# Performance work log

Hardware: AMD Instinct MI355X
Metric: run time of the kernel (lower is better)

The kernel has to match this reference:

```python
import jax, jax.numpy as jnp
import numpy as np

HUGE = 1e31  # ops.HUGE_INT
EPS = 1e-20

NUM_ENT, NUM_REL = 100000, 400
ENT_D, REL_D, HIST_D = 256, 256, 512
ACT_D = ENT_D + REL_D          # 512
IN_D = ENT_D + HIST_D + REL_D  # 1024
B, A = 512, 256


def setup_inputs() -> dict:
    key = jax.random.key(0)
    ks = jax.random.split(key, 10)
    s = 0.02
    return {
        "current_entity": jax.random.randint(ks[0], (B,), 0, NUM_ENT),
        "query_relation": jax.random.randint(ks[1], (B,), 0, NUM_REL),
        "encoded_history": jax.random.normal(ks[2], (B, HIST_D), jnp.float32),
        "r_space": jax.random.randint(ks[3], (B, A), 0, NUM_REL),
        "e_space": jax.random.randint(ks[4], (B, A), 0, NUM_ENT),
        "action_mask": jax.random.randint(ks[5], (B, A), 0, 2).astype(jnp.int32),
        "entity_emb": jax.random.normal(ks[6], (NUM_ENT, ENT_D), jnp.float32) * s,
        "relation_emb": jax.random.normal(ks[7], (NUM_REL, REL_D), jnp.float32) * s,
        "W1": jax.random.normal(ks[8], (IN_D, ACT_D), jnp.float32) * s,
        "b1": jnp.zeros((ACT_D,), jnp.float32),
        "W2": jax.random.normal(ks[9], (ACT_D, ACT_D), jnp.float32) * s,
        "b2": jnp.zeros((ACT_D,), jnp.float32),
    }


def reference(current_entity, query_relation, encoded_history, r_space, e_space,
              action_mask, entity_emb, relation_emb, W1, b1, W2, b2):
    # encode_history: [E(cur) | lstm hidden | R(query)] -> [B, IN_D]
    X = jnp.concatenate([entity_emb[current_entity], encoded_history,
                         relation_emb[query_relation]], axis=-1)
    # policy MLP (dropout = identity in eval)
    X2 = jax.nn.relu(X @ W1 + b1) @ W2 + b2          # [B, ACT_D]
    # per-action embeddings: concat(rel, ent) -> [B, A, ACT_D]
    A_emb = jnp.concatenate([relation_emb[r_space], entity_emb[e_space]], axis=-1)
    mask = action_mask.astype(X2.dtype)
    scores = jnp.einsum('bad,bd->ba', A_emb, X2) - (1.0 - mask) * HUGE
    action_dist = jax.nn.softmax(scores, axis=-1)    # [B, A]
    entropy = -jnp.sum(action_dist * jnp.log(action_dist + EPS), axis=-1)  # [B]
    return action_dist, entropy
```

## Files before the change

kernel.cpp:

```cpp
#include <hip/hip_runtime.h>
#include <hip/hip_bf16.h>

#define ENT_D 256
#define REL_D 256
#define HIST_D 512
#define ACT_DD 512
#define IN_DD 1024
#define BB 512
#define AA 256

typedef short bf16x8 __attribute__((ext_vector_type(8)));
typedef float floatx4 __attribute__((ext_vector_type(4)));

__device__ __forceinline__ unsigned short f2bf(float f) {
    unsigned u = __builtin_bit_cast(unsigned, f);
    return (unsigned short)((u + 0x7fffu + ((u >> 16) & 1u)) >> 16);
}


__global__ __launch_bounds__(256) void pack_kernel(
    const int* __restrict__ cur, const int* __restrict__ qrel,
    const float* __restrict__ hist,
    const float* __restrict__ ent_emb, const float* __restrict__ rel_emb,
    const float* __restrict__ W1, const float* __restrict__ W2,
    unsigned short* __restrict__ W1p, unsigned short* __restrict__ W2p,
    unsigned short* __restrict__ Xp)
{
    const int wid  = blockIdx.x * 4 + (threadIdx.x >> 6);
    const int lane = threadIdx.x & 63;
    const int l15  = lane & 15;
    const int quad = lane >> 4;
    unsigned short v[8];

    if (wid < 1024) {
        const int t = wid, nt = t >> 5, kt = t & 31;
        const int n = nt * 16 + l15, k0 = kt * 32 + quad * 8;
#pragma unroll
        for (int j = 0; j < 8; ++j) v[j] = f2bf(W1[(size_t)(k0 + j) * ACT_DD + n]);
        *(bf16x8*)(W1p + ((size_t)t * 64 + lane) * 8) = *(bf16x8*)v;
    } else if (wid < 1536) {
        const int t = wid - 1024, nt = t >> 4, kt = t & 15;
        const int n = nt * 16 + l15, k0 = kt * 32 + quad * 8;
#pragma unroll
        for (int j = 0; j < 8; ++j) v[j] = f2bf(W2[(size_t)(k0 + j) * ACT_DD + n]);
        *(bf16x8*)(W2p + ((size_t)t * 64 + lane) * 8) = *(bf16x8*)v;
    } else {
        const int t = wid - 1536, mt = t >> 5, kt = t & 31;
        const int m = mt * 16 + l15, k0 = kt * 32 + quad * 8;
        const float* src;
        if (k0 < ENT_D)            src = ent_emb + (size_t)cur[m] * ENT_D + k0;
        else if (k0 < ENT_D + HIST_D) src = hist + (size_t)m * HIST_D + (k0 - ENT_D);
        else                       src = rel_emb + (size_t)qrel[m] * REL_D + (k0 - ENT_D - HIST_D);
        float4 a = *(const float4*)src, b = *(const float4*)(src + 4);
        v[0]=f2bf(a.x); v[1]=f2bf(a.y); v[2]=f2bf(a.z); v[3]=f2bf(a.w);
        v[4]=f2bf(b.x); v[5]=f2bf(b.y); v[6]=f2bf(b.z); v[7]=f2bf(b.w);
        *(bf16x8*)(Xp + ((size_t)t * 64 + lane) * 8) = *(bf16x8*)v;
    }
}

__global__ __launch_bounds__(256) void gemm1_kernel(
    const unsigned short* __restrict__ Xp, const unsigned short* __restrict__ W1p,
    const float* __restrict__ b1, unsigned short* __restrict__ Hp)
{
    __shared__ unsigned short sH[1024];
    const int mt = blockIdx.x, wave = threadIdx.x >> 6, lane = threadIdx.x & 63;
    const int nt = blockIdx.y * 4 + wave;

    const bf16x8* Av = (const bf16x8*)Xp  + (size_t)mt * 32 * 64 + lane;
    const bf16x8* Bv = (const bf16x8*)W1p + (size_t)nt * 32 * 64 + lane;
    floatx4 acc = {0.f, 0.f, 0.f, 0.f};
#pragma unroll 8
    for (int kt = 0; kt < 32; ++kt)
        acc = __builtin_amdgcn_mfma_f32_16x16x32_bf16(Av[kt * 64], Bv[kt * 64], acc, 0, 0, 0);

    const int col  = nt * 16 + (lane & 15);
    const float bj = b1[col];
    const int n_loc = wave * 16 + (lane & 15);
    const int tile_loc = n_loc >> 5, quad2 = (n_loc & 31) >> 3, j2 = n_loc & 7;
#pragma unroll
    for (int reg = 0; reg < 4; ++reg) {
        const int row = (lane >> 4) * 4 + reg;
        const float h = fmaxf(acc[reg] + bj, 0.f);
        sH[tile_loc * 512 + (row + 16 * quad2) * 8 + j2] = f2bf(h);
    }
    __syncthreads();
    const int h = threadIdx.x * 4;
    const int tl = h >> 9, rest = h & 511;
    const size_t dst = ((size_t)(mt * 16 + blockIdx.y * 2 + tl) * 512 + rest);
    *(uint2*)(Hp + dst) = *(const uint2*)(sH + h);
}

__global__ __launch_bounds__(256) void gemm2_kernel(
    const unsigned short* __restrict__ Hp, const unsigned short* __restrict__ W2p,
    const float* __restrict__ b2, float* __restrict__ X2)
{
    const int mt = blockIdx.x, wave = threadIdx.x >> 6, lane = threadIdx.x & 63;
    const int nt = blockIdx.y * 4 + wave;

    const bf16x8* Av = (const bf16x8*)Hp  + (size_t)mt * 16 * 64 + lane;
    const bf16x8* Bv = (const bf16x8*)W2p + (size_t)nt * 16 * 64 + lane;
    floatx4 acc = {0.f, 0.f, 0.f, 0.f};
#pragma unroll
    for (int kt = 0; kt < 16; ++kt)
        acc = __builtin_amdgcn_mfma_f32_16x16x32_bf16(Av[kt * 64], Bv[kt * 64], acc, 0, 0, 0);

    const int col = nt * 16 + (lane & 15);
    const float bj = b2[col];
#pragma unroll
    for (int reg = 0; reg < 4; ++reg) {
        const int m = mt * 16 + (lane >> 4) * 4 + reg;
        X2[(size_t)m * ACT_DD + col] = acc[reg] + bj;
    }
}

__global__ __launch_bounds__(256) void score_kernel(
    const float* __restrict__ X2,
    const int* __restrict__ r_space, const int* __restrict__ e_space,
    const int* __restrict__ amask,
    const float* __restrict__ ent_emb, const float* __restrict__ rel_emb,
    float* __restrict__ scores)
{
    __shared__ __align__(16) float x2s[ACT_DD];
    const int b = blockIdx.x >> 2, chunk = blockIdx.x & 3;
    const int tid = threadIdx.x, wave = tid >> 6, lane = tid & 63;

    x2s[tid]       = X2[(size_t)b * ACT_DD + tid];
    x2s[tid + 256] = X2[(size_t)b * ACT_DD + tid + 256];
    __syncthreads();

    const float4 xr = ((const float4*)&x2s[0])[lane];
    const float4 xe = ((const float4*)&x2s[REL_D])[lane];
    const int a0 = chunk * 64 + wave * 16;

#pragma unroll
    for (int g = 0; g < 4; ++g) {
        const int ab = a0 + g * 4;
        int ir[4], ie[4];
        float p[4];
#pragma unroll
        for (int i = 0; i < 4; ++i) {
            ir[i] = r_space[b * AA + ab + i];
            ie[i] = e_space[b * AA + ab + i];
        }
#pragma unroll
        for (int i = 0; i < 4; ++i) {
            const float4 r4 = ((const float4*)(rel_emb + (size_t)ir[i] * REL_D))[lane];
            const float4 e4 = ((const float4*)(ent_emb + (size_t)ie[i] * ENT_D))[lane];
            p[i] = r4.x * xr.x + r4.y * xr.y + r4.z * xr.z + r4.w * xr.w
                 + e4.x * xe.x + e4.y * xe.y + e4.z * xe.z + e4.w * xe.w;
        }
#pragma unroll
        for (int off = 32; off > 0; off >>= 1) {
#pragma unroll
            for (int i = 0; i < 4; ++i) p[i] += __shfl_xor(p[i], off, 64);
        }
        if (lane == 0) {
#pragma unroll
            for (int i = 0; i < 4; ++i) {
                const float m = (float)amask[b * AA + ab + i];
                scores[(size_t)b * AA + ab + i] = p[i] - (1.0f - m) * 1e31f;
            }
        }
    }
}

__global__ __launch_bounds__(256) void softmax_kernel(
    const float* __restrict__ scores, float* __restrict__ dist, float* __restrict__ ent_out)
{
    __shared__ float red[4];
    const int b = blockIdx.x, tid = threadIdx.x, wave = tid >> 6, lane = tid & 63;
    const float s = scores[(size_t)b * AA + tid];

    float v = s;
#pragma unroll
    for (int off = 32; off > 0; off >>= 1) v = fmaxf(v, __shfl_xor(v, off, 64));
    if (lane == 0) red[wave] = v;
    __syncthreads();
    const float mx = fmaxf(fmaxf(red[0], red[1]), fmaxf(red[2], red[3]));
    __syncthreads();

    const float e = __expf(s - mx);
    v = e;
#pragma unroll
    for (int off = 32; off > 0; off >>= 1) v += __shfl_xor(v, off, 64);
    if (lane == 0) red[wave] = v;
    __syncthreads();
    const float sum = red[0] + red[1] + red[2] + red[3];
    __syncthreads();

    const float p = e / sum;
    dist[(size_t)b * AA + tid] = p;

    v = p * __logf(p + 1e-20f);
#pragma unroll
    for (int off = 32; off > 0; off >>= 1) v += __shfl_xor(v, off, 64);
    if (lane == 0) red[wave] = v;
    __syncthreads();
    if (tid == 0) ent_out[b] = -(red[0] + red[1] + red[2] + red[3]);
}

extern "C" void kernel_launch(void* const* d_in, const int* in_sizes, int n_in,
                              void* d_out, int out_size, void* d_ws, size_t ws_size,
                              hipStream_t stream) {
    const int*   cur      = (const int*)d_in[0];
    const int*   qrel     = (const int*)d_in[1];
    const float* hist     = (const float*)d_in[2];
    const int*   r_space  = (const int*)d_in[3];
    const int*   e_space  = (const int*)d_in[4];
    const int*   amask    = (const int*)d_in[5];
    const float* ent_emb  = (const float*)d_in[6];
    const float* rel_emb  = (const float*)d_in[7];
    const float* W1       = (const float*)d_in[8];
    const float* b1       = (const float*)d_in[9];
    const float* W2       = (const float*)d_in[10];
    const float* b2       = (const float*)d_in[11];

    float* dist    = (float*)d_out;
    float* entropy = dist + (size_t)BB * AA;

    char* w = (char*)d_ws;
    unsigned short* W1p = (unsigned short*)(w);
    unsigned short* W2p = (unsigned short*)(w + (1u << 20));
    unsigned short* Xp  = (unsigned short*)(w + (3u << 19));
    float*          scores = (float*)(w + (3u << 19));
    unsigned short* Hp  = (unsigned short*)(w + (5u << 19));
    float*          X2  = (float*)(w + (6u << 19));

    pack_kernel<<<640, 256, 0, stream>>>(cur, qrel, hist, ent_emb, rel_emb, W1, W2, W1p, W2p, Xp);
    gemm1_kernel<<<dim3(32, 8), 256, 0, stream>>>(Xp, W1p, b1, Hp);
    gemm2_kernel<<<dim3(32, 8), 256, 0, stream>>>(Hp, W2p, b2, X2);
    score_kernel<<<2048, 256, 0, stream>>>(X2, r_space, e_space, amask, ent_emb, rel_emb, scores);
    softmax_kernel<<<512, 256, 0, stream>>>(scores, dist, entropy);
}
```

Before: 193.7 us.

## Fuse score gather and softmax into one per-row kernel with deeper load batching

Merges the score and softmax kernels into one kernel with one 512-thread block per batch row. Scores stay in shared memory instead of going out to a global buffer, which saves a kernel launch and a global round trip. Each wave now issues 8 rel and 8 ent row gathers before any arithmetic, so more memory requests are in flight. In exchange the grid shrinks from 2048 to 512 blocks and the softmax phase leaves half the threads idle.

```diff
diff --git a/kernel.cpp b/kernel.cpp
--- a/kernel.cpp
+++ b/kernel.cpp
@@ -113,90 +113,100 @@
     }
 }
 
-__global__ __launch_bounds__(256) void score_kernel(
+__global__ __launch_bounds__(512) void score_softmax_kernel(
     const float* __restrict__ X2,
     const int* __restrict__ r_space, const int* __restrict__ e_space,
     const int* __restrict__ amask,
     const float* __restrict__ ent_emb, const float* __restrict__ rel_emb,
-    float* __restrict__ scores)
+    float* __restrict__ dist, float* __restrict__ ent_out)
 {
     __shared__ __align__(16) float x2s[ACT_DD];
-    const int b = blockIdx.x >> 2, chunk = blockIdx.x & 3;
-    const int tid = threadIdx.x, wave = tid >> 6, lane = tid & 63;
-
-    x2s[tid]       = X2[(size_t)b * ACT_DD + tid];
-    x2s[tid + 256] = X2[(size_t)b * ACT_DD + tid + 256];
+    __shared__ float sc[AA];
+    __shared__ float red[8];
+
+    const int b = blockIdx.x, tid = threadIdx.x;
+    const int wave = tid >> 6, lane = tid & 63;
+
+    x2s[tid] = X2[(size_t)b * ACT_DD + tid];
     __syncthreads();
 
     const float4 xr = ((const float4*)&x2s[0])[lane];
     const float4 xe = ((const float4*)&x2s[REL_D])[lane];
-    const int a0 = chunk * 64 + wave * 16;
 
 #pragma unroll
     for (int g = 0; g < 4; ++g) {
-        const int ab = a0 + g * 4;
-        int ir[4], ie[4];
-        float p[4];
-#pragma unroll
-        for (int i = 0; i < 4; ++i) {
+        const int ab = wave * 32 + g * 8;
+        int ir[8], ie[8];
+#pragma unroll
+        for (int i = 0; i < 8; ++i) {
             ir[i] = r_space[b * AA + ab + i];
             ie[i] = e_space[b * AA + ab + i];
         }
-#pragma unroll
-        for (int i = 0; i < 4; ++i) {
-            const float4 r4 = ((const float4*)(rel_emb + (size_t)ir[i] * REL_D))[lane];
-            const float4 e4 = ((const float4*)(ent_emb + (size_t)ie[i] * ENT_D))[lane];
-            p[i] = r4.x * xr.x + r4.y * xr.y + r4.z * xr.z + r4.w * xr.w
-                 + e4.x * xe.x + e4.y * xe.y + e4.z * xe.z + e4.w * xe.w;
-        }
+        float4 r4[8], e4[8];
+#pragma unroll
+        for (int i = 0; i < 8; ++i)
+            r4[i] = ((const float4*)(rel_emb + (size_t)ir[i] * REL_D))[lane];
+#pragma unroll
+        for (int i = 0; i < 8; ++i)
+            e4[i] = ((const float4*)(ent_emb + (size_t)ie[i] * ENT_D))[lane];
+
+        float p[8];
+#pragma unroll
+        for (int i = 0; i < 8; ++i)
+            p[i] = r4[i].x * xr.x + r4[i].y * xr.y + r4[i].z * xr.z + r4[i].w * xr.w
+                 + e4[i].x * xe.x + e4[i].y * xe.y + e4[i].z * xe.z + e4[i].w * xe.w;
 #pragma unroll
         for (int off = 32; off > 0; off >>= 1) {
 #pragma unroll
-            for (int i = 0; i < 4; ++i) p[i] += __shfl_xor(p[i], off, 64);
+            for (int i = 0; i < 8; ++i) p[i] += __shfl_xor(p[i], off, 64);
         }
         if (lane == 0) {
 #pragma unroll
-            for (int i = 0; i < 4; ++i) {
-                const float m = (float)amask[b * AA + ab + i];
-                scores[(size_t)b * AA + ab + i] = p[i] - (1.0f - m) * 1e31f;
-            }
+            for (int i = 0; i < 8; ++i) sc[ab + i] = p[i];
         }
     }
-}
-
-__global__ __launch_bounds__(256) void softmax_kernel(
-    const float* __restrict__ scores, float* __restrict__ dist, float* __restrict__ ent_out)
-{
-    __shared__ float red[4];
-    const int b = blockIdx.x, tid = threadIdx.x, wave = tid >> 6, lane = tid & 63;
-    const float s = scores[(size_t)b * AA + tid];
-
+    __syncthreads();
+
+    float s = -3.0e38f;
+    if (tid < AA) {
+        const float m = (float)amask[b * AA + tid];
+        s = sc[tid] - (1.0f - m) * 1e31f;
+    }
     float v = s;
 #pragma unroll
     for (int off = 32; off > 0; off >>= 1) v = fmaxf(v, __shfl_xor(v, off, 64));
     if (lane == 0) red[wave] = v;
     __syncthreads();
-    const float mx = fmaxf(fmaxf(red[0], red[1]), fmaxf(red[2], red[3]));
-    __syncthreads();
-
-    const float e = __expf(s - mx);
+    float mx = red[0];
+#pragma unroll
+    for (int w = 1; w < 8; ++w) mx = fmaxf(mx, red[w]);
+    __syncthreads();
+
+    const float e = (tid < AA) ? __expf(s - mx) : 0.0f;
     v = e;
 #pragma unroll
     for (int off = 32; off > 0; off >>= 1) v += __shfl_xor(v, off, 64);
     if (lane == 0) red[wave] = v;
     __syncthreads();
-    const float sum = red[0] + red[1] + red[2] + red[3];
+    float sum = red[0];
+#pragma unroll
+    for (int w = 1; w < 8; ++w) sum += red[w];
     __syncthreads();
 
     const float p = e / sum;
-    dist[(size_t)b * AA + tid] = p;
-
-    v = p * __logf(p + 1e-20f);
+    if (tid < AA) dist[(size_t)b * AA + tid] = p;
+
+    v = (tid < AA) ? p * __logf(p + 1e-20f) : 0.0f;
 #pragma unroll
     for (int off = 32; off > 0; off >>= 1) v += __shfl_xor(v, off, 64);
     if (lane == 0) red[wave] = v;
     __syncthreads();
-    if (tid == 0) ent_out[b] = -(red[0] + red[1] + red[2] + red[3]);
+    if (tid == 0) {
+        float t = red[0];
+#pragma unroll
+        for (int w = 1; w < 8; ++w) t += red[w];
+        ent_out[b] = -t;
+    }
 }
 
 extern "C" void kernel_launch(void* const* d_in, const int* in_sizes, int n_in,
@@ -222,13 +232,12 @@
     unsigned short* W1p = (unsigned short*)(w);
     unsigned short* W2p = (unsigned short*)(w + (1u << 20));
     unsigned short* Xp  = (unsigned short*)(w + (3u << 19));
-    float*          scores = (float*)(w + (3u << 19));
     unsigned short* Hp  = (unsigned short*)(w + (5u << 19));
     float*          X2  = (float*)(w + (6u << 19));
 
     pack_kernel<<<640, 256, 0, stream>>>(cur, qrel, hist, ent_emb, rel_emb, W1, W2, W1p, W2p, Xp);
     gemm1_kernel<<<dim3(32, 8), 256, 0, stream>>>(Xp, W1p, b1, Hp);
     gemm2_kernel<<<dim3(32, 8), 256, 0, stream>>>(Hp, W2p, b2, X2);
-    score_kernel<<<2048, 256, 0, stream>>>(X2, r_space, e_space, amask, ent_emb, rel_emb, scores);
-    softmax_kernel<<<512, 256, 0, stream>>>(scores, dist, entropy);
-}
+    score_softmax_kernel<<<512, 512, 0, stream>>>(X2, r_space, e_space, amask,
+                                                  ent_emb, rel_emb, dist, entropy);
+}
```

After: 189.6 us. -2.1%, faster.
